# Kernel tuning notes

Measured on AMD Instinct MI355X. Metric: run time of the kernel, lower is better.

The kernel has to match this reference:

```python
import jax, jax.numpy as jnp
import numpy as np
import math

# Model hyperparameters (SchNet defaults)
H = 128        # hidden_channels
F = 128        # num_filters
G = 50         # num_gaussians
CUT = 6.0      # cutoff (Angstrom)
L_INT = 3      # num_interactions
# Graph scale
N_MOL = 512    # molecules
APM = 32       # atoms per molecule
N = N_MOL * APM
BOX = 10.0     # side of cubic box per molecule


def _ssp(x):
    # ShiftedSoftplus
    return jax.nn.softplus(x) - math.log(2.0)


def setup_inputs() -> dict:
    rng = np.random.default_rng(0)
    pos = rng.uniform(0.0, BOX, (N_MOL, APM, 3)).astype(np.float32)
    # radius graph within each molecule (faithful to radius_graph_custom,
    # precomputed here because edge count is data-dependent)
    srcs, dsts = [], []
    for m in range(N_MOL):
        p = pos[m]
        dm = np.linalg.norm(p[:, None, :] - p[None, :, :], axis=-1)
        mask = dm <= CUT
        np.fill_diagonal(mask, False)
        s, t = np.nonzero(mask)
        srcs.append(s + m * APM)
        dsts.append(t + m * APM)
    edge_index = np.stack([np.concatenate(srcs), np.concatenate(dsts)]).astype(np.int32)
    pos = pos.reshape(N, 3)
    batch = np.repeat(np.arange(N_MOL, dtype=np.int32), APM)
    z = rng.integers(1, 100, N).astype(np.int32)

    key = jax.random.key(0)
    ks = jax.random.split(key, 16)
    s = 0.1
    nrm = lambda k, shp: (jax.random.normal(k, shp, dtype=jnp.float32) * s)
    return {
        "z": jnp.asarray(z),
        "pos": jnp.asarray(pos),
        "batch": jnp.asarray(batch),
        "edge_index": jnp.asarray(edge_index),
        "emb": nrm(ks[0], (100, H)),
        "mlp_w1": nrm(ks[1], (L_INT, G, F)),
        "mlp_b1": jnp.zeros((L_INT, F), jnp.float32),
        "mlp_w2": nrm(ks[2], (L_INT, F, F)),
        "mlp_b2": jnp.zeros((L_INT, F), jnp.float32),
        "cf1_w": nrm(ks[3], (L_INT, H, F)),
        "cf2_w": nrm(ks[4], (L_INT, F, H)),
        "cf2_b": jnp.zeros((L_INT, H), jnp.float32),
        "lin_w": nrm(ks[5], (L_INT, H, H)),
        "lin_b": jnp.zeros((L_INT, H), jnp.float32),
        "out1_w": nrm(ks[6], (H, H // 2)),
        "out1_b": jnp.zeros((H // 2,), jnp.float32),
        "out2_w": nrm(ks[7], (H // 2, 1)),
        "out2_b": jnp.zeros((1,), jnp.float32),
    }


def reference(z, pos, batch, edge_index, emb,
              mlp_w1, mlp_b1, mlp_w2, mlp_b2,
              cf1_w, cf2_w, cf2_b, lin_w, lin_b,
              out1_w, out1_b, out2_w, out2_b):
    src, dst = edge_index[0], edge_index[1]
    # edge_weight = euclidean distance (== cdist[src, dst])
    d = jnp.sqrt(jnp.sum((pos[src] - pos[dst]) ** 2, axis=-1))  # [E]
    # GaussianSmearing
    offs = jnp.linspace(0.0, CUT, G)
    coeff = -0.5 / (CUT / (G - 1)) ** 2
    edge_attr = jnp.exp(coeff * (d[:, None] - offs[None, :]) ** 2)  # [E, G]
    # cosine cutoff
    Ccut = 0.5 * (jnp.cos(d * math.pi / CUT) + 1.0)  # [E]

    h = emb[z]  # [N, H]
    for l in range(L_INT):
        # edge filter MLP with cutoff
        W = _ssp(edge_attr @ mlp_w1[l] + mlp_b1[l]) @ mlp_w2[l] + mlp_b2[l]  # [E, F]
        W = W * Ccut[:, None]
        # CFConv: lin1 -> gather x_j -> multiply -> scatter-add to dst -> lin2
        msg = (h @ cf1_w[l])[src] * W                                # [E, F]
        agg = jax.ops.segment_sum(msg, dst, num_segments=N)          # [N, F]
        v = agg @ cf2_w[l] + cf2_b[l]                                # [N, H]
        v = _ssp(v)
        v = v @ lin_w[l] + lin_b[l]
        h = h + v  # residual

    h = _ssp(h @ out1_w + out1_b)
    h = h @ out2_w + out2_b                                          # [N, 1]
    out = jax.ops.segment_sum(h, batch, num_segments=N_MOL)          # [N_MOL, 1]
    return out
```

## Files before the change

kernel.cpp:

```cpp
#include <hip/hip_runtime.h>
#include <hip/hip_bf16.h>
#include <math.h>

#define NATOMS 16384
#define NMOL   512
#define APM    32
#define GDIM   50
#define KTAB   4096

#define STRH 132
#define STRA 136

typedef __attribute__((ext_vector_type(8))) short   short8;
typedef __attribute__((ext_vector_type(4))) float   floatx4;

__device__ __forceinline__ float ssp(float x) {
    float e = __expf(-fabsf(x));
    return fmaxf(x, 0.0f) + __logf(1.0f + e) - 0.69314718055994531f;
}

__device__ __forceinline__ unsigned short f2bf(float x) {
    union { float f; unsigned int u; } v; v.f = x;
    unsigned int lsb = (v.u >> 16) & 1u;
    v.u += 0x7fffu + lsb;
    return (unsigned short)(v.u >> 16);
}

__device__ __forceinline__ unsigned int pk2bf(float a, float b) {
    __hip_bfloat162 h = __float22bfloat162_rn(make_float2(a, b));
    unsigned int u;
    __builtin_memcpy(&u, &h, 4);
    return u;
}

#define KW1 72
#define KW2 136
#define NTILE (KTAB / 64)

__global__ __launch_bounds__(256) void mega_setup_kernel(
    const float* __restrict__ pos,
    unsigned* __restrict__ koG,
    const float* __restrict__ cf1, const float* __restrict__ cf2,
    const float* __restrict__ lin, const float* __restrict__ out1,
    unsigned short* __restrict__ Wtall,
    const float* __restrict__ w1_, const float* __restrict__ b1_,
    const float* __restrict__ w2_, const float* __restrict__ b2_,
    unsigned short* __restrict__ Tt)
{
    const int WB = (9 * 16384 + 64 * 128 + 255) / 256;
    const int b = blockIdx.x;
    const int tid = threadIdx.x;

    __shared__ float sp[96];

    if (b < NMOL) {
        if (tid < 96) sp[tid] = pos[b * 96 + tid];
        if (b < 3 && tid < 128)
            Tt[(size_t)b * (KTAB + 1) * 128 + (size_t)KTAB * 128 + tid] = 0;
        __syncthreads();
        #pragma unroll
        for (int c4 = 0; c4 < 4; c4++) {
            int c = c4 * 256 + tid;
            int i = c >> 5, j = c & 31;
            float dx = sp[3 * i]     - sp[3 * j];
            float dy = sp[3 * i + 1] - sp[3 * j + 1];
            float dz = sp[3 * i + 2] - sp[3 * j + 2];
            float d  = sqrtf(dx * dx + dy * dy + dz * dz);
            unsigned off = (unsigned)(KTAB << 8);
            if (i != j && d <= 6.0f) {
                float u = d * (float)(KTAB - 1) / 6.0f;
                int k = min((int)(u + 0.5f), KTAB - 1);
                off = (unsigned)(k << 8);
            }
            koG[((size_t)b << 10) + c] = off;
        }
        return;
    }
    if (b < NMOL + WB) {
        int idx = (b - NMOL) * 256 + tid;
        if (idx < 9 * 16384) {
            int wi = idx >> 14, rem = idx & 16383;
            int n = rem >> 7, k = rem & 127;
            int l = wi / 3, which = wi % 3;
            const float* src = (which == 0) ? cf1 : (which == 1) ? cf2 : lin;
            Wtall[idx] = f2bf(src[(size_t)l * 16384 + k * 128 + n]);
        } else if (idx < 9 * 16384 + 64 * 128) {
            int q = idx - 9 * 16384;
            int n = q >> 7, k = q & 127;
            Wtall[idx] = f2bf(out1[k * 64 + n]);
        }
        return;
    }

    __shared__ unsigned short s_bufA[128 * KW2];
    __shared__ unsigned short s_bufB[128 * KW1];

    const int tt = b - NMOL - WB;
    const int l  = tt / NTILE;
    const int bx = tt % NTILE;
    const float* w1 = w1_ + (size_t)l * GDIM * 128;
    const float* b1 = b1_ + (size_t)l * 128;
    const float* w2 = w2_ + (size_t)l * 128 * 128;
    const float* b2 = b2_ + (size_t)l * 128;
    unsigned short* Tg = Tt + (size_t)l * (KTAB + 1) * 128;

    unsigned short* s_w1T = s_bufB;
    unsigned short* s_w2T = s_bufA;
    unsigned short* s_t   = s_bufB;

    for (int i = tid; i < GDIM * 128; i += 256) {
        int g = i >> 7, f = i & 127;
        s_w1T[f * KW1 + g] = f2bf(w1[i]);
    }
    for (int i = tid; i < (64 - GDIM) * 128; i += 256) {
        int g = GDIM + (i >> 7), f = i & 127;
        s_w1T[f * KW1 + g] = 0;
    }
    for (int i = tid; i < 128 * 128; i += 256) {
        int k = i >> 7, n = i & 127;
        s_w2T[n * KW2 + k] = f2bf(w2[i]);
    }

    const int lane = tid & 63;
    const int w    = tid >> 6;
    const int l15  = lane & 15;
    const int quad = lane >> 4;

    float b1v[8], b2v[8];
    #pragma unroll
    for (int nt = 0; nt < 8; nt++) {
        b1v[nt] = b1[nt * 16 + l15];
        b2v[nt] = b2[nt * 16 + l15];
    }
    __syncthreads();

    const float hstep = 6.0f / (float)(KTAB - 1);
    const float step  = 6.0f / 49.0f;
    const float coeff = -0.5f / (step * step);
    const float pioc  = 3.14159265358979323846f / 6.0f;
    const int k0 = bx * 64;
    const float dm = (float)(k0 + w * 16 + l15) * hstep;

    floatx4 acc1[8];
    #pragma unroll
    for (int nt = 0; nt < 8; nt++) acc1[nt] = (floatx4){0.f, 0.f, 0.f, 0.f};
    #pragma unroll
    for (int ks = 0; ks < 2; ks++) {
        unsigned int ap[4];
        #pragma unroll
        for (int jj = 0; jj < 4; jj++) {
            int g0 = ks * 32 + quad * 8 + 2 * jj;
            float d0 = dm - (float)g0 * step;
            float d1 = dm - (float)(g0 + 1) * step;
            float v0 = (g0 < GDIM)     ? __expf(coeff * d0 * d0) : 0.0f;
            float v1 = (g0 + 1 < GDIM) ? __expf(coeff * d1 * d1) : 0.0f;
            ap[jj] = pk2bf(v0, v1);
        }
        short8 af;
        __builtin_memcpy(&af, ap, 16);
        #pragma unroll
        for (int nt = 0; nt < 8; nt++) {
            short8 bfg = *(const short8*)&s_w1T[(nt * 16 + l15) * KW1 + ks * 32 + quad * 8];
            acc1[nt] = __builtin_amdgcn_mfma_f32_16x16x32_bf16(af, bfg, acc1[nt], 0, 0, 0);
        }
    }
    __syncthreads();

    #pragma unroll
    for (int nt = 0; nt < 8; nt++) {
        #pragma unroll
        for (int r = 0; r < 4; r++) {
            int row = w * 16 + quad * 4 + r;
            s_t[row * KW2 + nt * 16 + l15] = f2bf(ssp(acc1[nt][r] + b1v[nt]));
        }
    }

    floatx4 acc2[8];
    #pragma unroll
    for (int nt = 0; nt < 8; nt++) acc2[nt] = (floatx4){0.f, 0.f, 0.f, 0.f};
    #pragma unroll
    for (int ks = 0; ks < 4; ks++) {
        short8 af = *(const short8*)&s_t[(w * 16 + l15) * KW2 + ks * 32 + quad * 8];
        #pragma unroll
        for (int nt = 0; nt < 8; nt++) {
            short8 bfg = *(const short8*)&s_w2T[(nt * 16 + l15) * KW2 + ks * 32 + quad * 8];
            acc2[nt] = __builtin_amdgcn_mfma_f32_16x16x32_bf16(af, bfg, acc2[nt], 0, 0, 0);
        }
    }

    #pragma unroll
    for (int nt = 0; nt < 8; nt++) {
        #pragma unroll
        for (int r = 0; r < 4; r++) {
            int row = w * 16 + quad * 4 + r;
            float d = (float)(k0 + row) * hstep;
            float cut = 0.5f * (__cosf(d * pioc) + 1.0f);
            Tg[(size_t)(k0 + row) * 128 + nt * 16 + l15] = f2bf((acc2[nt][r] + b2v[nt]) * cut);
        }
    }
}

__global__ __launch_bounds__(512, 4) void fused_schnet_kernel(
    const int* __restrict__ z, const float* __restrict__ emb,
    const unsigned* __restrict__ koG,
    const unsigned short* __restrict__ Tt,
    const unsigned short* __restrict__ Wtall,
    const float* __restrict__ cf2_b, const float* __restrict__ lin_b,
    const float* __restrict__ out1_b, const float* __restrict__ out2_w,
    const float* __restrict__ out2_b,
    float* __restrict__ out)
{
    __shared__ float s_h[32 * STRH];
    __shared__ float s_hx[32 * 128];
    __shared__ unsigned short s_agg[32 * STRA];
    __shared__ unsigned int s_ko[32 * 32];
    __shared__ float s_red;
    unsigned short* s_t = (unsigned short*)s_hx;

    const int tid  = threadIdx.x;
    const int lane = tid & 63;
    const int w    = tid >> 6;
    const int l15  = lane & 15;
    const int quad = lane >> 4;
    const int r16  = (w & 1) * 16;
    const int c32  = (w >> 1) * 32;
    const int B0   = blockIdx.x * 32;

    const unsigned lOff = (unsigned)(lane << 2);

    for (int i = tid; i < 32 * 128; i += 512) {
        int row = i >> 7, col = i & 127;
        s_h[row * STRH + col] = emb[(size_t)z[B0 + row] * 128 + col];
    }
    for (int i = tid; i < 1024; i += 512)
        s_ko[i] = koG[((size_t)blockIdx.x << 10) + i];
    if (tid == 0) s_red = 0.0f;

    __syncthreads();

    const unsigned short* WtO = Wtall + 9 * 16384;

#define KO_RFL(KO, SC)                                                        \
    _Pragma("unroll")                                                         \
    for (int i = 0; i < 4; i++) {                                             \
        uint4 ka = *(const uint4*)&s_ko[(((w << 2) + i) << 5) + ((SC) << 3)]; \
        uint4 kb = *(const uint4*)&s_ko[(((w << 2) + i) << 5) + ((SC) << 3) + 4]; \
        KO[i][0] = __builtin_amdgcn_readfirstlane(ka.x);                      \
        KO[i][1] = __builtin_amdgcn_readfirstlane(ka.y);                      \
        KO[i][2] = __builtin_amdgcn_readfirstlane(ka.z);                      \
        KO[i][3] = __builtin_amdgcn_readfirstlane(ka.w);                      \
        KO[i][4] = __builtin_amdgcn_readfirstlane(kb.x);                      \
        KO[i][5] = __builtin_amdgcn_readfirstlane(kb.y);                      \
        KO[i][6] = __builtin_amdgcn_readfirstlane(kb.z);                      \
        KO[i][7] = __builtin_amdgcn_readfirstlane(kb.w);                      \
    }
#define TP_LOAD(TP, KO)                                                       \
    _Pragma("unroll")                                                         \
    for (int i = 0; i < 4; i++) {                                             \
        _Pragma("unroll")                                                     \
        for (int j = 0; j < 8; j++)                                           \
            TP[i][j] = *(const unsigned*)(TlB + KO[i][j] + lOff);             \
    }
#define FMA_CHUNK(TP, SC)                                                     \
    _Pragma("unroll")                                                         \
    for (int j = 0; j < 8; j++) {                                             \
        float2 hv = *(const float2*)&s_hx[((((SC) << 3) + j) << 7) + (lane << 1)]; \
        _Pragma("unroll")                                                     \
        for (int i = 0; i < 4; i++) {                                         \
            unsigned t = TP[i][j];                                            \
            a0[i] = fmaf(hv.x, __uint_as_float(t << 16),         a0[i]);      \
            a1[i] = fmaf(hv.y, __uint_as_float(t & 0xffff0000u), a1[i]);      \
        }                                                                     \
    }

    for (int l = 0; l < 3; l++) {
        const unsigned short* W1 = Wtall + (size_t)(l * 3 + 0) * 16384;
        const unsigned short* W2 = Wtall + (size_t)(l * 3 + 1) * 16384;
        const unsigned short* W3 = Wtall + (size_t)(l * 3 + 2) * 16384;
        const char* TlB = (const char*)(Tt + (size_t)l * (KTAB + 1) * 128);

        unsigned koA[4][8], koB[4][8], tpA[4][8], tpB[4][8];
        KO_RFL(koA, 0)
        TP_LOAD(tpA, koA)

        __syncthreads();

        floatx4 acc[2];
        #pragma unroll
        for (int nt = 0; nt < 2; nt++) acc[nt] = (floatx4){0.f, 0.f, 0.f, 0.f};
        #pragma unroll
        for (int ks = 0; ks < 4; ks++) {
            const float* hp = &s_h[(r16 + l15) * STRH + ks * 32 + quad * 8];
            float4 xa = *(const float4*)hp;
            float4 xb = *(const float4*)(hp + 4);
            unsigned int ap[4];
            ap[0] = pk2bf(xa.x, xa.y); ap[1] = pk2bf(xa.z, xa.w);
            ap[2] = pk2bf(xb.x, xb.y); ap[3] = pk2bf(xb.z, xb.w);
            short8 af;
            __builtin_memcpy(&af, ap, 16);
            #pragma unroll
            for (int nt = 0; nt < 2; nt++) {
                short8 bfg = *(const short8*)&W1[(size_t)(c32 + nt * 16 + l15) * 128 + ks * 32 + quad * 8];
                acc[nt] = __builtin_amdgcn_mfma_f32_16x16x32_bf16(af, bfg, acc[nt], 0, 0, 0);
            }
        }
        #pragma unroll
        for (int nt = 0; nt < 2; nt++) {
            #pragma unroll
            for (int r = 0; r < 4; r++)
                s_hx[(r16 + quad * 4 + r) * 128 + c32 + nt * 16 + l15] = acc[nt][r];
        }

        __syncthreads();

        {
            float a0[4], a1[4];
            #pragma unroll
            for (int i = 0; i < 4; i++) { a0[i] = 0.0f; a1[i] = 0.0f; }

            KO_RFL(koB, 1)
            TP_LOAD(tpB, koB)
            FMA_CHUNK(tpA, 0)

            KO_RFL(koA, 2)
            TP_LOAD(tpA, koA)
            FMA_CHUNK(tpB, 1)

            KO_RFL(koB, 3)
            TP_LOAD(tpB, koB)
            FMA_CHUNK(tpA, 2)

            FMA_CHUNK(tpB, 3)

            #pragma unroll
            for (int i = 0; i < 4; i++)
                *(unsigned*)&s_agg[((w << 2) + i) * STRA + (lane << 1)] = pk2bf(a0[i], a1[i]);
        }

        __syncthreads();

        float bva[2], bvb[2];
        #pragma unroll
        for (int nt = 0; nt < 2; nt++) {
            bva[nt] = cf2_b[l * 128 + c32 + nt * 16 + l15];
            bvb[nt] = lin_b[l * 128 + c32 + nt * 16 + l15];
        }
        #pragma unroll
        for (int nt = 0; nt < 2; nt++) acc[nt] = (floatx4){0.f, 0.f, 0.f, 0.f};
        #pragma unroll
        for (int ks = 0; ks < 4; ks++) {
            short8 af = *(const short8*)&s_agg[(r16 + l15) * STRA + ks * 32 + quad * 8];
            #pragma unroll
            for (int nt = 0; nt < 2; nt++) {
                short8 bfg = *(const short8*)&W2[(size_t)(c32 + nt * 16 + l15) * 128 + ks * 32 + quad * 8];
                acc[nt] = __builtin_amdgcn_mfma_f32_16x16x32_bf16(af, bfg, acc[nt], 0, 0, 0);
            }
        }
        #pragma unroll
        for (int nt = 0; nt < 2; nt++) {
            #pragma unroll
            for (int r = 0; r < 4; r++) {
                int row = r16 + quad * 4 + r;
                s_t[row * STRA + c32 + nt * 16 + l15] = f2bf(ssp(acc[nt][r] + bva[nt]));
            }
        }

        __syncthreads();

        #pragma unroll
        for (int nt = 0; nt < 2; nt++) acc[nt] = (floatx4){0.f, 0.f, 0.f, 0.f};
        #pragma unroll
        for (int ks = 0; ks < 4; ks++) {
            short8 af = *(const short8*)&s_t[(r16 + l15) * STRA + ks * 32 + quad * 8];
            #pragma unroll
            for (int nt = 0; nt < 2; nt++) {
                short8 bfg = *(const short8*)&W3[(size_t)(c32 + nt * 16 + l15) * 128 + ks * 32 + quad * 8];
                acc[nt] = __builtin_amdgcn_mfma_f32_16x16x32_bf16(af, bfg, acc[nt], 0, 0, 0);
            }
        }
        #pragma unroll
        for (int nt = 0; nt < 2; nt++) {
            #pragma unroll
            for (int r = 0; r < 4; r++) {
                int row = r16 + quad * 4 + r;
                s_h[row * STRH + c32 + nt * 16 + l15] += acc[nt][r] + bvb[nt];
            }
        }
    }

    __syncthreads();

    const int c16 = (w >> 1) * 16;
    floatx4 ha = (floatx4){0.f, 0.f, 0.f, 0.f};
    #pragma unroll
    for (int ks = 0; ks < 4; ks++) {
        const float* hp = &s_h[(r16 + l15) * STRH + ks * 32 + quad * 8];
        float4 xa = *(const float4*)hp;
        float4 xb = *(const float4*)(hp + 4);
        unsigned int ap[4];
        ap[0] = pk2bf(xa.x, xa.y); ap[1] = pk2bf(xa.z, xa.w);
        ap[2] = pk2bf(xb.x, xb.y); ap[3] = pk2bf(xb.z, xb.w);
        short8 af;
        __builtin_memcpy(&af, ap, 16);
        short8 bfg = *(const short8*)&WtO[(size_t)(c16 + l15) * 128 + ks * 32 + quad * 8];
        ha = __builtin_amdgcn_mfma_f32_16x16x32_bf16(af, bfg, ha, 0, 0, 0);
    }
    float part = 0.0f;
    {
        float b1o = out1_b[c16 + l15];
        float o2  = out2_w[c16 + l15];
        #pragma unroll
        for (int r = 0; r < 4; r++)
            part += ssp(ha[r] + b1o) * o2;
    }
    #pragma unroll
    for (int off = 32; off > 0; off >>= 1) part += __shfl_down(part, off);
    if (lane == 0) atomicAdd(&s_red, part);
    __syncthreads();
    if (tid == 0) out[blockIdx.x] = s_red + 32.0f * out2_b[0];

#undef KO_RFL
#undef TP_LOAD
#undef FMA_CHUNK
}

extern "C" void kernel_launch(void* const* d_in, const int* in_sizes, int n_in,
                              void* d_out, int out_size, void* d_ws, size_t ws_size,
                              hipStream_t stream)
{
    const int*   z      = (const int*)d_in[0];
    const float* pos    = (const float*)d_in[1];
    const float* emb    = (const float*)d_in[4];
    const float* mlp_w1 = (const float*)d_in[5];
    const float* mlp_b1 = (const float*)d_in[6];
    const float* mlp_w2 = (const float*)d_in[7];
    const float* mlp_b2 = (const float*)d_in[8];
    const float* cf1_w  = (const float*)d_in[9];
    const float* cf2_w  = (const float*)d_in[10];
    const float* cf2_b  = (const float*)d_in[11];
    const float* lin_w  = (const float*)d_in[12];
    const float* lin_b  = (const float*)d_in[13];
    const float* out1_w = (const float*)d_in[14];
    const float* out1_b = (const float*)d_in[15];
    const float* out2_w = (const float*)d_in[16];
    const float* out2_b = (const float*)d_in[17];

    char* p = (char*)d_ws;
    unsigned* koG = (unsigned*)p;                 p += (size_t)NMOL * 1024 * 4;
    unsigned short* Tt = (unsigned short*)p;      p += (size_t)3 * (KTAB + 1) * 128 * 2;
    unsigned short* Wtall = (unsigned short*)p;

    const int WB = (9 * 16384 + 64 * 128 + 255) / 256;
    const int TB = NTILE * 3;
    mega_setup_kernel<<<NMOL + WB + TB, 256, 0, stream>>>(
        pos, koG, cf1_w, cf2_w, lin_w, out1_w, Wtall,
        mlp_w1, mlp_b1, mlp_w2, mlp_b2, Tt);

    fused_schnet_kernel<<<NMOL, 512, 0, stream>>>(
        z, emb, koG, Tt, Wtall,
        cf2_b, lin_b, out1_b, out2_w, out2_b, (float*)d_out);
}
```

Baseline: 161.4 us.

## Store filter table in fp32 and use packed FMA in edge aggregation

The precomputed distance-indexed filter table changes from bf16 to fp32, so the per-edge gather reads float2 directly and uses packed fp32 FMA instead of bf16 unpacking. The manual software pipeline of table loads and readfirstlane offsets is replaced by a plain unrolled loop left to the compiler. A barrier moves inside the layer loop. The table doubles in size (about 6 MB), so gathers carry more cache and memory traffic, and dropping the explicit prefetch may expose load latency.

```diff
diff --git a/kernel.cpp b/kernel.cpp
--- a/kernel.cpp
+++ b/kernel.cpp
@@ -13,6 +13,7 @@
 
 typedef __attribute__((ext_vector_type(8))) short   short8;
 typedef __attribute__((ext_vector_type(4))) float   floatx4;
+typedef __attribute__((ext_vector_type(2))) float   floatx2;
 
 __device__ __forceinline__ float ssp(float x) {
     float e = __expf(-fabsf(x));
@@ -45,7 +46,7 @@
     unsigned short* __restrict__ Wtall,
     const float* __restrict__ w1_, const float* __restrict__ b1_,
     const float* __restrict__ w2_, const float* __restrict__ b2_,
-    unsigned short* __restrict__ Tt)
+    float* __restrict__ Tt)
 {
     const int WB = (9 * 16384 + 64 * 128 + 255) / 256;
     const int b = blockIdx.x;
@@ -56,7 +57,7 @@
     if (b < NMOL) {
         if (tid < 96) sp[tid] = pos[b * 96 + tid];
         if (b < 3 && tid < 128)
-            Tt[(size_t)b * (KTAB + 1) * 128 + (size_t)KTAB * 128 + tid] = 0;
+            Tt[(size_t)b * (KTAB + 1) * 128 + (size_t)KTAB * 128 + tid] = 0.0f;
         __syncthreads();
         #pragma unroll
         for (int c4 = 0; c4 < 4; c4++) {
@@ -66,11 +67,11 @@
             float dy = sp[3 * i + 1] - sp[3 * j + 1];
             float dz = sp[3 * i + 2] - sp[3 * j + 2];
             float d  = sqrtf(dx * dx + dy * dy + dz * dz);
-            unsigned off = (unsigned)(KTAB << 8);
+            unsigned off = (unsigned)(KTAB << 9);
             if (i != j && d <= 6.0f) {
                 float u = d * (float)(KTAB - 1) / 6.0f;
                 int k = min((int)(u + 0.5f), KTAB - 1);
-                off = (unsigned)(k << 8);
+                off = (unsigned)(k << 9);
             }
             koG[((size_t)b << 10) + c] = off;
         }
@@ -102,7 +103,7 @@
     const float* b1 = b1_ + (size_t)l * 128;
     const float* w2 = w2_ + (size_t)l * 128 * 128;
     const float* b2 = b2_ + (size_t)l * 128;
-    unsigned short* Tg = Tt + (size_t)l * (KTAB + 1) * 128;
+    float* Tg = Tt + (size_t)l * (KTAB + 1) * 128;
 
     unsigned short* s_w1T = s_bufB;
     unsigned short* s_w2T = s_bufA;
@@ -195,7 +196,7 @@
             int row = w * 16 + quad * 4 + r;
             float d = (float)(k0 + row) * hstep;
             float cut = 0.5f * (__cosf(d * pioc) + 1.0f);
-            Tg[(size_t)(k0 + row) * 128 + nt * 16 + l15] = f2bf((acc2[nt][r] + b2v[nt]) * cut);
+            Tg[(size_t)(k0 + row) * 128 + nt * 16 + l15] = (acc2[nt][r] + b2v[nt]) * cut;
         }
     }
 }
@@ -203,7 +204,7 @@
 __global__ __launch_bounds__(512, 4) void fused_schnet_kernel(
     const int* __restrict__ z, const float* __restrict__ emb,
     const unsigned* __restrict__ koG,
-    const unsigned short* __restrict__ Tt,
+    const float* __restrict__ Tt,
     const unsigned short* __restrict__ Wtall,
     const float* __restrict__ cf2_b, const float* __restrict__ lin_b,
     const float* __restrict__ out1_b, const float* __restrict__ out2_w,
@@ -226,7 +227,7 @@
     const int c32  = (w >> 1) * 32;
     const int B0   = blockIdx.x * 32;
 
-    const unsigned lOff = (unsigned)(lane << 2);
+    const unsigned lOff = (unsigned)(lane << 3);
 
     for (int i = tid; i < 32 * 128; i += 512) {
         int row = i >> 7, col = i & 127;
@@ -239,51 +240,12 @@
     __syncthreads();
 
     const unsigned short* WtO = Wtall + 9 * 16384;
-
-#define KO_RFL(KO, SC)                                                        \
-    _Pragma("unroll")                                                         \
-    for (int i = 0; i < 4; i++) {                                             \
-        uint4 ka = *(const uint4*)&s_ko[(((w << 2) + i) << 5) + ((SC) << 3)]; \
-        uint4 kb = *(const uint4*)&s_ko[(((w << 2) + i) << 5) + ((SC) << 3) + 4]; \
-        KO[i][0] = __builtin_amdgcn_readfirstlane(ka.x);                      \
-        KO[i][1] = __builtin_amdgcn_readfirstlane(ka.y);                      \
-        KO[i][2] = __builtin_amdgcn_readfirstlane(ka.z);                      \
-        KO[i][3] = __builtin_amdgcn_readfirstlane(ka.w);                      \
-        KO[i][4] = __builtin_amdgcn_readfirstlane(kb.x);                      \
-        KO[i][5] = __builtin_amdgcn_readfirstlane(kb.y);                      \
-        KO[i][6] = __builtin_amdgcn_readfirstlane(kb.z);                      \
-        KO[i][7] = __builtin_amdgcn_readfirstlane(kb.w);                      \
-    }
-#define TP_LOAD(TP, KO)                                                       \
-    _Pragma("unroll")                                                         \
-    for (int i = 0; i < 4; i++) {                                             \
-        _Pragma("unroll")                                                     \
-        for (int j = 0; j < 8; j++)                                           \
-            TP[i][j] = *(const unsigned*)(TlB + KO[i][j] + lOff);             \
-    }
-#define FMA_CHUNK(TP, SC)                                                     \
-    _Pragma("unroll")                                                         \
-    for (int j = 0; j < 8; j++) {                                             \
-        float2 hv = *(const float2*)&s_hx[((((SC) << 3) + j) << 7) + (lane << 1)]; \
-        _Pragma("unroll")                                                     \
-        for (int i = 0; i < 4; i++) {                                         \
-            unsigned t = TP[i][j];                                            \
-            a0[i] = fmaf(hv.x, __uint_as_float(t << 16),         a0[i]);      \
-            a1[i] = fmaf(hv.y, __uint_as_float(t & 0xffff0000u), a1[i]);      \
-        }                                                                     \
-    }
 
     for (int l = 0; l < 3; l++) {
         const unsigned short* W1 = Wtall + (size_t)(l * 3 + 0) * 16384;
         const unsigned short* W2 = Wtall + (size_t)(l * 3 + 1) * 16384;
         const unsigned short* W3 = Wtall + (size_t)(l * 3 + 2) * 16384;
         const char* TlB = (const char*)(Tt + (size_t)l * (KTAB + 1) * 128);
-
-        unsigned koA[4][8], koB[4][8], tpA[4][8], tpB[4][8];
-        KO_RFL(koA, 0)
-        TP_LOAD(tpA, koA)
-
-        __syncthreads();
 
         floatx4 acc[2];
         #pragma unroll
@@ -314,27 +276,33 @@
         __syncthreads();
 
         {
-            float a0[4], a1[4];
-            #pragma unroll
-            for (int i = 0; i < 4; i++) { a0[i] = 0.0f; a1[i] = 0.0f; }
-
-            KO_RFL(koB, 1)
-            TP_LOAD(tpB, koB)
-            FMA_CHUNK(tpA, 0)
-
-            KO_RFL(koA, 2)
-            TP_LOAD(tpA, koA)
-            FMA_CHUNK(tpB, 1)
-
-            KO_RFL(koB, 3)
-            TP_LOAD(tpB, koB)
-            FMA_CHUNK(tpA, 2)
-
-            FMA_CHUNK(tpB, 3)
-
+            floatx2 av[4];
+            #pragma unroll
+            for (int i = 0; i < 4; i++) av[i] = (floatx2){0.f, 0.f};
+
+            #pragma unroll
+            for (int sc = 0; sc < 4; sc++) {
+                unsigned ko[4][8];
+                #pragma unroll
+                for (int i = 0; i < 4; i++) {
+                    uint4 ka = *(const uint4*)&s_ko[(((w << 2) + i) << 5) + (sc << 3)];
+                    uint4 kb = *(const uint4*)&s_ko[(((w << 2) + i) << 5) + (sc << 3) + 4];
+                    ko[i][0] = ka.x; ko[i][1] = ka.y; ko[i][2] = ka.z; ko[i][3] = ka.w;
+                    ko[i][4] = kb.x; ko[i][5] = kb.y; ko[i][6] = kb.z; ko[i][7] = kb.w;
+                }
+                #pragma unroll
+                for (int j = 0; j < 8; j++) {
+                    floatx2 hv = *(const floatx2*)&s_hx[(((sc << 3) + j) << 7) + (lane << 1)];
+                    #pragma unroll
+                    for (int i = 0; i < 4; i++) {
+                        floatx2 tp = *(const floatx2*)(TlB + (ko[i][j] + lOff));
+                        av[i] = __builtin_elementwise_fma(tp, hv, av[i]);
+                    }
+                }
+            }
             #pragma unroll
             for (int i = 0; i < 4; i++)
-                *(unsigned*)&s_agg[((w << 2) + i) * STRA + (lane << 1)] = pk2bf(a0[i], a1[i]);
+                *(unsigned*)&s_agg[((w << 2) + i) * STRA + (lane << 1)] = pk2bf(av[i].x, av[i].y);
         }
 
         __syncthreads();
@@ -386,9 +354,8 @@
                 s_h[row * STRH + c32 + nt * 16 + l15] += acc[nt][r] + bvb[nt];
             }
         }
-    }
-
-    __syncthreads();
+        __syncthreads();
+    }
 
     const int c16 = (w >> 1) * 16;
     floatx4 ha = (floatx4){0.f, 0.f, 0.f, 0.f};
@@ -418,10 +385,6 @@
     if (lane == 0) atomicAdd(&s_red, part);
     __syncthreads();
     if (tid == 0) out[blockIdx.x] = s_red + 32.0f * out2_b[0];
-
-#undef KO_RFL
-#undef TP_LOAD
-#undef FMA_CHUNK
 }
 
 extern "C" void kernel_launch(void* const* d_in, const int* in_sizes, int n_in,
@@ -447,7 +410,7 @@
 
     char* p = (char*)d_ws;
     unsigned* koG = (unsigned*)p;                 p += (size_t)NMOL * 1024 * 4;
-    unsigned short* Tt = (unsigned short*)p;      p += (size_t)3 * (KTAB + 1) * 128 * 2;
+    float* Tt = (float*)p;                        p += (size_t)3 * (KTAB + 1) * 128 * 4;
     unsigned short* Wtall = (unsigned short*)p;
 
     const int WB = (9 * 16384 + 64 * 128 + 255) / 256;
```

New measurement: 188.5 us. +16.8%, slower.
